# Kernel tuning notes

Measured on AMD Instinct MI355X. Metric: run time of the kernel, lower is better.

Reference implementation:

```python
import jax, jax.numpy as jnp
import numpy as np

EPS = 1e-12


def setup_inputs() -> dict:
    key = jax.random.key(0)
    N, C, H, W = 32, 256, 56, 56
    k1, k2, k3 = jax.random.split(key, 3)
    x = jax.random.normal(k1, (N, C, H, W), dtype=jnp.float32)
    weight = 1.0 + 0.1 * jax.random.normal(k2, (C,), dtype=jnp.float32)
    bias = 0.1 * jax.random.normal(k3, (C,), dtype=jnp.float32)
    # Variable group sizes summing to C=256 (16 groups)
    gs = np.array([8, 24, 8, 16, 32, 16, 8, 8, 16, 24, 8, 16, 16, 8, 32, 16], dtype=np.int64)
    assert gs.sum() == C
    # Per-sample channel permutation expressed as row indices into x.view(N*C, H*W)
    rng = np.random.default_rng(0)
    perms = np.stack([rng.permutation(C) for _ in range(N)])  # [N, C]
    offs = np.arange(N)[:, None] * C
    indexes = (perms + offs).reshape(-1).astype(np.int64)
    inv = np.argsort(perms, axis=1)
    reverse_indexes = (inv + offs).reshape(-1).astype(np.int64)
    return {
        "x": x,
        "weight": weight,
        "bias": bias,
        "group_sizes": jnp.asarray(gs),
        "indexes": jnp.asarray(indexes),
        "reverse_indexes": jnp.asarray(reverse_indexes),
    }


def reference(x, weight, bias, group_sizes, indexes, reverse_indexes):
    N, C, H, W = x.shape
    HW = H * W
    gs = np.asarray(group_sizes)          # static group layout
    G = gs.shape[0]
    seg = jnp.asarray(np.repeat(np.arange(G), gs))  # [C] channel -> group id
    n = jnp.asarray(gs * HW, dtype=x.dtype)         # [G] elements per group

    # gather: per-sample channel permutation
    xg = x.reshape(N * C, HW)[indexes].reshape(N, C, HW)

    # per-group mean via segmented reduction over channels
    s1 = xg.sum(axis=2)                                    # [N, C]
    mu_g = jax.ops.segment_sum(s1.T, seg, num_segments=G).T / n      # [N, G]
    mu_c = mu_g[:, seg]                                    # [N, C]

    diff = xg - mu_c[:, :, None]
    s2 = (diff * diff).sum(axis=2)                         # [N, C]
    # torch.var default is unbiased -> divide by (n - 1)
    var_g = jax.ops.segment_sum(s2.T, seg, num_segments=G).T / (n - 1.0)
    ivar_c = (1.0 / jnp.sqrt(var_g + EPS))[:, seg]         # [N, C]

    out = diff * ivar_c[:, :, None] * weight[None, :, None] + bias[None, :, None]

    # scatter back to original channel order
    out = out.reshape(N * C, HW)[reverse_indexes].reshape(N, C, H, W)
    return out
```

## Files before the change

### kernel.cpp

```cpp
#include <hip/hip_runtime.h>

#define N_ 32
#define C_ 256
#define G_ 16
#define HW_ 3136
#define HW4_ 784
#define EPS_ 1e-12f

typedef float vf4 __attribute__((ext_vector_type(4)));
typedef float vf2 __attribute__((ext_vector_type(2)));

__device__ __forceinline__ int rd_int(const int* __restrict__ p, int i, bool is64) {
    return is64 ? p[2 * i] : p[i];
}

__device__ __forceinline__ void acc4(const vf4 v, float& s, float& s2) {
    s += v.x + v.y + v.z + v.w;
    s2 = fmaf(v.x, v.x, s2);
    s2 = fmaf(v.y, v.y, s2);
    s2 = fmaf(v.z, v.z, s2);
    s2 = fmaf(v.w, v.w, s2);
}

__device__ __forceinline__ vf4 aff(const vf4 v, float sc, float sh) {
    vf4 r;
    r.x = fmaf(v.x, sc, sh);
    r.y = fmaf(v.y, sc, sh);
    r.z = fmaf(v.z, sc, sh);
    r.w = fmaf(v.w, sc, sh);
    return r;
}


__global__ __launch_bounds__(256, 8) void vgn_reduce(
    const float* __restrict__ x,
    const int*   __restrict__ indexes,
    const int*   __restrict__ group_sizes,
    float*       __restrict__ rsums)
{
    const bool is64 = (group_sizes[1] == 0);
    const int t  = threadIdx.x;
    const int r0 = blockIdx.x * 2;

    const int src0 = rd_int(indexes, r0,     is64);
    const int src1 = rd_int(indexes, r0 + 1, is64);
    const vf4* p0 = (const vf4*)x + (size_t)src0 * HW4_;
    const vf4* p1 = (const vf4*)x + (size_t)src1 * HW4_;

    vf4 a0 = p0[t], b0 = p0[t + 256], c0 = p0[t + 512];
    vf4 a1 = p1[t], b1 = p1[t + 256], c1 = p1[t + 512];

    float sA = 0.f, qA = 0.f, sB = 0.f, qB = 0.f;
    if (t < 16) {
        vf4 d0 = p0[768 + t];
        vf4 d1 = p1[768 + t];
        acc4(d0, sA, qA);
        acc4(d1, sB, qB);
    }
    acc4(a0, sA, qA); acc4(b0, sA, qA); acc4(c0, sA, qA);
    acc4(a1, sB, qB); acc4(b1, sB, qB); acc4(c1, sB, qB);

    #pragma unroll
    for (int off = 32; off > 0; off >>= 1) {
        sA += __shfl_down(sA, off);
        qA += __shfl_down(qA, off);
        sB += __shfl_down(sB, off);
        qB += __shfl_down(qB, off);
    }

    __shared__ float red[4][4];
    if ((t & 63) == 0) {
        const int w = t >> 6;
        red[w][0] = sA; red[w][1] = qA; red[w][2] = sB; red[w][3] = qB;
    }
    __syncthreads();
    if (t < 4)
        rsums[r0 * 2 + t] = red[0][t] + red[1][t] + red[2][t] + red[3][t];
}

__global__ __launch_bounds__(256, 8) void vgn_norm(
    const float* __restrict__ x,
    const int*   __restrict__ indexes,
    const int*   __restrict__ group_sizes,
    const float* __restrict__ weight,
    const float* __restrict__ bias,
    const float* __restrict__ rsums,
    float*       __restrict__ out)
{
    const bool is64 = (group_sizes[1] == 0);
    const int t  = threadIdx.x;
    const int r0 = blockIdx.x * 2;
    const int n  = r0 >> 8;

    const int src0 = rd_int(indexes, r0,     is64);
    const int src1 = rd_int(indexes, r0 + 1, is64);
    const vf4* p0 = (const vf4*)x + (size_t)src0 * HW4_;
    const vf4* p1 = (const vf4*)x + (size_t)src1 * HW4_;
    vf4* o0 = (vf4*)out + (size_t)src0 * HW4_;
    vf4* o1 = (vf4*)out + (size_t)src1 * HW4_;

    vf4 a0 = p0[t], b0 = p0[t + 256], c0 = p0[t + 512];
    vf4 a1 = p1[t], b1 = p1[t + 256], c1 = p1[t + 512];
    vf4 d0, d1;
    const bool tail = (t < 16);
    if (tail) { d0 = p0[768 + t]; d1 = p1[768 + t]; }

    __shared__ float sScale[2], sShift[2];
    if (t < 64) {
        const int half = t >> 5;
        const int l    = t & 31;
        const int j    = (r0 + half) & 255;
        int g = 0, P = 0, Pg = 0;
        #pragma unroll
        for (int k = 0; k < G_; k++) {
            P += rd_int(group_sizes, k, is64);
            if (j >= P) { g++; Pg = P; }
        }
        const int gsz = rd_int(group_sizes, g, is64);
        float a = 0.f, b = 0.f;
        if (l < gsz) {
            const vf2 pr = ((const vf2*)rsums)[n * C_ + Pg + l];
            a = pr.x; b = pr.y;
        }
        #pragma unroll
        for (int off = 16; off > 0; off >>= 1) {
            a += __shfl_down(a, off, 32);
            b += __shfl_down(b, off, 32);
        }
        if (l == 0) {
            const float cnt = (float)gsz * (float)HW_;
            const float mu  = a / cnt;
            const float var = (b - mu * a) / (cnt - 1.0f);
            const float ivr = rsqrtf(var + EPS_);
            const float sc  = ivr * weight[j];
            sScale[half] = sc;
            sShift[half] = fmaf(-mu, sc, bias[j]);
        }
    }
    __syncthreads();

    const float sc0 = sScale[0], sh0 = sShift[0];
    const float sc1 = sScale[1], sh1 = sShift[1];

    o0[t]       = aff(a0, sc0, sh0);
    o0[t + 256] = aff(b0, sc0, sh0);
    o0[t + 512] = aff(c0, sc0, sh0);
    o1[t]       = aff(a1, sc1, sh1);
    o1[t + 256] = aff(b1, sc1, sh1);
    o1[t + 512] = aff(c1, sc1, sh1);
    if (tail) {
        o0[768 + t] = aff(d0, sc0, sh0);
        o1[768 + t] = aff(d1, sc1, sh1);
    }
}

extern "C" void kernel_launch(void* const* d_in, const int* in_sizes, int n_in,
                              void* d_out, int out_size, void* d_ws, size_t ws_size,
                              hipStream_t stream) {
    const float* x           = (const float*)d_in[0];
    const float* weight      = (const float*)d_in[1];
    const float* bias        = (const float*)d_in[2];
    const int*   group_sizes = (const int*)  d_in[3];
    const int*   indexes     = (const int*)  d_in[4];

    float* rsums = (float*)d_ws;

    dim3 grid(N_ * C_ / 2), block(256);
    vgn_reduce<<<grid, block, 0, stream>>>(x, indexes, group_sizes, rsums);
    vgn_norm  <<<grid, block, 0, stream>>>(x, indexes, group_sizes,
                                           weight, bias, rsums, (float*)d_out);
}
```

Baseline: 201.9 us.

## Process rows in source order and move group stats into a small kernel

The reduce and normalize kernels now walk x rows contiguously in their original order rather than through the permuted index gather. A new small vgn_stats kernel maps each group's member channels to their source rows via indexes, reduces the per-row sums, and writes per-row scale and shift. The normalize kernel then just loads its two precomputed coefficients. This removes the scattered row access and the per-block group search, at the cost of one more kernel launch.

```diff
diff --git a/kernel.cpp b/kernel.cpp
--- a/kernel.cpp
+++ b/kernel.cpp
@@ -34,18 +34,13 @@
 
 __global__ __launch_bounds__(256, 8) void vgn_reduce(
     const float* __restrict__ x,
-    const int*   __restrict__ indexes,
-    const int*   __restrict__ group_sizes,
     float*       __restrict__ rsums)
 {
-    const bool is64 = (group_sizes[1] == 0);
     const int t  = threadIdx.x;
     const int r0 = blockIdx.x * 2;
 
-    const int src0 = rd_int(indexes, r0,     is64);
-    const int src1 = rd_int(indexes, r0 + 1, is64);
-    const vf4* p0 = (const vf4*)x + (size_t)src0 * HW4_;
-    const vf4* p1 = (const vf4*)x + (size_t)src1 * HW4_;
+    const vf4* p0 = (const vf4*)x + (size_t)r0 * HW4_;
+    const vf4* p1 = p0 + HW4_;
 
     vf4 a0 = p0[t], b0 = p0[t + 256], c0 = p0[t + 512];
     vf4 a1 = p1[t], b1 = p1[t + 256], c1 = p1[t + 512];
@@ -78,26 +73,65 @@
         rsums[r0 * 2 + t] = red[0][t] + red[1][t] + red[2][t] + red[3][t];
 }
 
-__global__ __launch_bounds__(256, 8) void vgn_norm(
-    const float* __restrict__ x,
+__global__ __launch_bounds__(64) void vgn_stats(
     const int*   __restrict__ indexes,
     const int*   __restrict__ group_sizes,
     const float* __restrict__ weight,
     const float* __restrict__ bias,
     const float* __restrict__ rsums,
+    float*       __restrict__ scaleS,
+    float*       __restrict__ shiftS)
+{
+    const bool is64 = (group_sizes[1] == 0);
+    const int n = blockIdx.x >> 4;
+    const int g = blockIdx.x & (G_ - 1);
+    const int l = threadIdx.x;
+
+    int Pg = 0;
+    for (int k = 0; k < g; k++) Pg += rd_int(group_sizes, k, is64);
+    const int gsz = rd_int(group_sizes, g, is64);
+
+    int src = 0;
+    float a = 0.f, b = 0.f;
+    if (l < gsz) {
+        src = rd_int(indexes, n * C_ + Pg + l, is64);
+        const vf2 pr = ((const vf2*)rsums)[src];
+        a = pr.x; b = pr.y;
+    }
+    float A = a, B = b;
+    #pragma unroll
+    for (int off = 32; off > 0; off >>= 1) {
+        A += __shfl_down(A, off);
+        B += __shfl_down(B, off);
+    }
+    A = __shfl(A, 0);
+    B = __shfl(B, 0);
+
+    if (l < gsz) {
+        const float cnt = (float)gsz * (float)HW_;
+        const float mu  = A / cnt;
+        const float var = (B - mu * A) / (cnt - 1.0f);
+        const float ivr = rsqrtf(var + EPS_);
+        const int   c   = Pg + l;
+        const float sc  = ivr * weight[c];
+        scaleS[src] = sc;
+        shiftS[src] = fmaf(-mu, sc, bias[c]);
+    }
+}
+
+__global__ __launch_bounds__(256, 8) void vgn_norm(
+    const float* __restrict__ x,
+    const float* __restrict__ scaleS,
+    const float* __restrict__ shiftS,
     float*       __restrict__ out)
 {
-    const bool is64 = (group_sizes[1] == 0);
     const int t  = threadIdx.x;
     const int r0 = blockIdx.x * 2;
-    const int n  = r0 >> 8;
 
-    const int src0 = rd_int(indexes, r0,     is64);
-    const int src1 = rd_int(indexes, r0 + 1, is64);
-    const vf4* p0 = (const vf4*)x + (size_t)src0 * HW4_;
-    const vf4* p1 = (const vf4*)x + (size_t)src1 * HW4_;
-    vf4* o0 = (vf4*)out + (size_t)src0 * HW4_;
-    vf4* o1 = (vf4*)out + (size_t)src1 * HW4_;
+    const vf4* p0 = (const vf4*)x + (size_t)r0 * HW4_;
+    const vf4* p1 = p0 + HW4_;
+    vf4* o0 = (vf4*)out + (size_t)r0 * HW4_;
+    vf4* o1 = o0 + HW4_;
 
     vf4 a0 = p0[t], b0 = p0[t + 256], c0 = p0[t + 512];
     vf4 a1 = p1[t], b1 = p1[t + 256], c1 = p1[t + 512];
@@ -105,42 +139,8 @@
     const bool tail = (t < 16);
     if (tail) { d0 = p0[768 + t]; d1 = p1[768 + t]; }
 
-    __shared__ float sScale[2], sShift[2];
-    if (t < 64) {
-        const int half = t >> 5;
-        const int l    = t & 31;
-        const int j    = (r0 + half) & 255;
-        int g = 0, P = 0, Pg = 0;
-        #pragma unroll
-        for (int k = 0; k < G_; k++) {
-            P += rd_int(group_sizes, k, is64);
-            if (j >= P) { g++; Pg = P; }
-        }
-        const int gsz = rd_int(group_sizes, g, is64);
-        float a = 0.f, b = 0.f;
-        if (l < gsz) {
-            const vf2 pr = ((const vf2*)rsums)[n * C_ + Pg + l];
-            a = pr.x; b = pr.y;
-        }
-        #pragma unroll
-        for (int off = 16; off > 0; off >>= 1) {
-            a += __shfl_down(a, off, 32);
-            b += __shfl_down(b, off, 32);
-        }
-        if (l == 0) {
-            const float cnt = (float)gsz * (float)HW_;
-            const float mu  = a / cnt;
-            const float var = (b - mu * a) / (cnt - 1.0f);
-            const float ivr = rsqrtf(var + EPS_);
-            const float sc  = ivr * weight[j];
-            sScale[half] = sc;
-            sShift[half] = fmaf(-mu, sc, bias[j]);
-        }
-    }
-    __syncthreads();
-
-    const float sc0 = sScale[0], sh0 = sShift[0];
-    const float sc1 = sScale[1], sh1 = sShift[1];
+    const float sc0 = scaleS[r0],     sh0 = shiftS[r0];
+    const float sc1 = scaleS[r0 + 1], sh1 = shiftS[r0 + 1];
 
     o0[t]       = aff(a0, sc0, sh0);
     o0[t + 256] = aff(b0, sc0, sh0);
@@ -163,10 +163,15 @@
     const int*   group_sizes = (const int*)  d_in[3];
     const int*   indexes     = (const int*)  d_in[4];
 
-    float* rsums = (float*)d_ws;
+    float* rsums  = (float*)d_ws;
+    float* scaleS = (float*)d_ws + 2 * N_ * C_;
+    float* shiftS = scaleS + N_ * C_;
+    float* outp   = (float*)d_out;
 
-    dim3 grid(N_ * C_ / 2), block(256);
-    vgn_reduce<<<grid, block, 0, stream>>>(x, indexes, group_sizes, rsums);
-    vgn_norm  <<<grid, block, 0, stream>>>(x, indexes, group_sizes,
-                                           weight, bias, rsums, (float*)d_out);
+    dim3 blkBulk(256), gridBulk(N_ * C_ / 2);
+    vgn_reduce<<<gridBulk, blkBulk, 0, stream>>>(x, rsums);
+    vgn_stats <<<dim3(N_ * G_), dim3(64), 0, stream>>>(indexes, group_sizes,
+                                                       weight, bias, rsums,
+                                                       scaleS, shiftS);
+    vgn_norm  <<<gridBulk, blkBulk, 0, stream>>>(x, scaleS, shiftS, outp);
 }
```

Measured after the change: 204.6 us. Within noise of the previous version (+1.4%).

## Fuse reduce and normalize into one pass with atomic group barriers

Applied to the files above, without the earlier changes.

Merges the two kernels into one. Each block reduces its two channels, adds the partial sums into per-group atomics, and spins on a flag until the last contributor of the group publishes mean and inverse std. The data stays in registers between reduction and normalization, so x is read once instead of twice. It adds a memset, atomics and spin-waits whose forward progress depends on every block of a group being resident at once.

```diff
diff --git a/kernel.cpp b/kernel.cpp
--- a/kernel.cpp
+++ b/kernel.cpp
@@ -5,10 +5,10 @@
 #define G_ 16
 #define HW_ 3136
 #define HW4_ 784
+#define NG_ (N_ * G_)
 #define EPS_ 1e-12f
 
 typedef float vf4 __attribute__((ext_vector_type(4)));
-typedef float vf2 __attribute__((ext_vector_type(2)));
 
 __device__ __forceinline__ int rd_int(const int* __restrict__ p, int i, bool is64) {
     return is64 ? p[2 * i] : p[i];
@@ -31,29 +31,51 @@
     return r;
 }
 
+__device__ __forceinline__ void vgn_release(
+    float* __restrict__ gS, float* __restrict__ gS2,
+    float* __restrict__ gMu, float* __restrict__ gIv,
+    int* __restrict__ gFlag, int gi, int gsz)
+{
+    const float S = atomicAdd(&gS[gi],  0.0f);
+    const float Q = atomicAdd(&gS2[gi], 0.0f);
+    const float cnt = (float)gsz * (float)HW_;
+    const float mu  = S / cnt;
+    const float var = (Q - mu * S) / (cnt - 1.0f);
+    const float iv  = rsqrtf(var + EPS_);
+    atomicExch(&gMu[gi], mu);
+    atomicExch(&gIv[gi], iv);
+    __threadfence();
+    atomicExch(&gFlag[gi], 1);
+}
 
-__global__ __launch_bounds__(256, 8) void vgn_reduce(
+__global__ __launch_bounds__(256, 8) void vgn_onepass(
     const float* __restrict__ x,
     const int*   __restrict__ indexes,
     const int*   __restrict__ group_sizes,
-    float*       __restrict__ rsums)
+    const float* __restrict__ weight,
+    const float* __restrict__ bias,
+    float* __restrict__ gS,   float* __restrict__ gS2,
+    float* __restrict__ gMu,  float* __restrict__ gIv,
+    int*   __restrict__ gCnt, int*   __restrict__ gFlag,
+    float* __restrict__ out)
 {
     const bool is64 = (group_sizes[1] == 0);
     const int t  = threadIdx.x;
-    const int r0 = blockIdx.x * 2;
+    const int n  = blockIdx.x >> 7;
+    const int p0 = (blockIdx.x & 127) * 2;
 
-    const int src0 = rd_int(indexes, r0,     is64);
-    const int src1 = rd_int(indexes, r0 + 1, is64);
-    const vf4* p0 = (const vf4*)x + (size_t)src0 * HW4_;
-    const vf4* p1 = (const vf4*)x + (size_t)src1 * HW4_;
+    const int src0 = rd_int(indexes, n * C_ + p0,     is64);
+    const int src1 = rd_int(indexes, n * C_ + p0 + 1, is64);
+    const vf4* q0 = (const vf4*)x + (size_t)src0 * HW4_;
+    const vf4* q1 = (const vf4*)x + (size_t)src1 * HW4_;
 
-    vf4 a0 = p0[t], b0 = p0[t + 256], c0 = p0[t + 512];
-    vf4 a1 = p1[t], b1 = p1[t + 256], c1 = p1[t + 512];
+    vf4 a0 = q0[t], b0 = q0[t + 256], c0 = q0[t + 512];
+    vf4 a1 = q1[t], b1 = q1[t + 256], c1 = q1[t + 512];
 
     float sA = 0.f, qA = 0.f, sB = 0.f, qB = 0.f;
     if (t < 16) {
-        vf4 d0 = p0[768 + t];
-        vf4 d1 = p1[768 + t];
+        vf4 d0 = q0[768 + t];
+        vf4 d1 = q1[768 + t];
         acc4(d0, sA, qA);
         acc4(d1, sB, qB);
     }
@@ -69,78 +91,65 @@
     }
 
     __shared__ float red[4][4];
+    __shared__ float sSc[2], sSh[2];
     if ((t & 63) == 0) {
         const int w = t >> 6;
         red[w][0] = sA; red[w][1] = qA; red[w][2] = sB; red[w][3] = qB;
     }
     __syncthreads();
-    if (t < 4)
-        rsums[r0 * 2 + t] = red[0][t] + red[1][t] + red[2][t] + red[3][t];
-}
 
-__global__ __launch_bounds__(256, 8) void vgn_norm(
-    const float* __restrict__ x,
-    const int*   __restrict__ indexes,
-    const int*   __restrict__ group_sizes,
-    const float* __restrict__ weight,
-    const float* __restrict__ bias,
-    const float* __restrict__ rsums,
-    float*       __restrict__ out)
-{
-    const bool is64 = (group_sizes[1] == 0);
-    const int t  = threadIdx.x;
-    const int r0 = blockIdx.x * 2;
-    const int n  = r0 >> 8;
+    if (t == 0) {
+        const float S0 = red[0][0] + red[1][0] + red[2][0] + red[3][0];
+        const float Q0 = red[0][1] + red[1][1] + red[2][1] + red[3][1];
+        const float S1 = red[0][2] + red[1][2] + red[2][2] + red[3][2];
+        const float Q1 = red[0][3] + red[1][3] + red[2][3] + red[3][3];
 
-    const int src0 = rd_int(indexes, r0,     is64);
-    const int src1 = rd_int(indexes, r0 + 1, is64);
-    const vf4* p0 = (const vf4*)x + (size_t)src0 * HW4_;
-    const vf4* p1 = (const vf4*)x + (size_t)src1 * HW4_;
-    vf4* o0 = (vf4*)out + (size_t)src0 * HW4_;
-    vf4* o1 = (vf4*)out + (size_t)src1 * HW4_;
-
-    vf4 a0 = p0[t], b0 = p0[t + 256], c0 = p0[t + 512];
-    vf4 a1 = p1[t], b1 = p1[t + 256], c1 = p1[t + 512];
-    vf4 d0, d1;
-    const bool tail = (t < 16);
-    if (tail) { d0 = p0[768 + t]; d1 = p1[768 + t]; }
-
-    __shared__ float sScale[2], sShift[2];
-    if (t < 64) {
-        const int half = t >> 5;
-        const int l    = t & 31;
-        const int j    = (r0 + half) & 255;
-        int g = 0, P = 0, Pg = 0;
+        int g0 = 0, g1 = 0, P = 0;
         #pragma unroll
         for (int k = 0; k < G_; k++) {
             P += rd_int(group_sizes, k, is64);
-            if (j >= P) { g++; Pg = P; }
+            if (p0     >= P) g0++;
+            if (p0 + 1 >= P) g1++;
         }
-        const int gsz = rd_int(group_sizes, g, is64);
-        float a = 0.f, b = 0.f;
-        if (l < gsz) {
-            const vf2 pr = ((const vf2*)rsums)[n * C_ + Pg + l];
-            a = pr.x; b = pr.y;
+        const int gsz0 = rd_int(group_sizes, g0, is64);
+        const int gsz1 = rd_int(group_sizes, g1, is64);
+        const int gi0 = n * G_ + g0;
+        const int gi1 = n * G_ + g1;
+
+        atomicAdd(&gS[gi0], S0);
+        atomicAdd(&gS2[gi0], Q0);
+        __threadfence();
+        if (atomicAdd(&gCnt[gi0], 1) == gsz0 - 1)
+            vgn_release(gS, gS2, gMu, gIv, gFlag, gi0, gsz0);
+
+        atomicAdd(&gS[gi1], S1);
+        atomicAdd(&gS2[gi1], Q1);
+        __threadfence();
+        if (atomicAdd(&gCnt[gi1], 1) == gsz1 - 1)
+            vgn_release(gS, gS2, gMu, gIv, gFlag, gi1, gsz1);
+
+        while (atomicAdd(&gFlag[gi0], 0) == 0) __builtin_amdgcn_s_sleep(2);
+        const float mu0 = atomicAdd(&gMu[gi0], 0.0f);
+        const float iv0 = atomicAdd(&gIv[gi0], 0.0f);
+        float mu1, iv1;
+        if (gi1 == gi0) { mu1 = mu0; iv1 = iv0; }
+        else {
+            while (atomicAdd(&gFlag[gi1], 0) == 0) __builtin_amdgcn_s_sleep(2);
+            mu1 = atomicAdd(&gMu[gi1], 0.0f);
+            iv1 = atomicAdd(&gIv[gi1], 0.0f);
         }
-        #pragma unroll
-        for (int off = 16; off > 0; off >>= 1) {
-            a += __shfl_down(a, off, 32);
-            b += __shfl_down(b, off, 32);
-        }
-        if (l == 0) {
-            const float cnt = (float)gsz * (float)HW_;
-            const float mu  = a / cnt;
-            const float var = (b - mu * a) / (cnt - 1.0f);
-            const float ivr = rsqrtf(var + EPS_);
-            const float sc  = ivr * weight[j];
-            sScale[half] = sc;
-            sShift[half] = fmaf(-mu, sc, bias[j]);
-        }
+
+        const float sc0 = iv0 * weight[p0];
+        const float sc1 = iv1 * weight[p0 + 1];
+        sSc[0] = sc0; sSh[0] = fmaf(-mu0, sc0, bias[p0]);
+        sSc[1] = sc1; sSh[1] = fmaf(-mu1, sc1, bias[p0 + 1]);
     }
     __syncthreads();
 
-    const float sc0 = sScale[0], sh0 = sShift[0];
-    const float sc1 = sScale[1], sh1 = sShift[1];
+    const float sc0 = sSc[0], sh0 = sSh[0];
+    const float sc1 = sSc[1], sh1 = sSh[1];
+    vf4* o0 = (vf4*)out + (size_t)src0 * HW4_;
+    vf4* o1 = (vf4*)out + (size_t)src1 * HW4_;
 
     o0[t]       = aff(a0, sc0, sh0);
     o0[t + 256] = aff(b0, sc0, sh0);
@@ -148,9 +157,9 @@
     o1[t]       = aff(a1, sc1, sh1);
     o1[t + 256] = aff(b1, sc1, sh1);
     o1[t + 512] = aff(c1, sc1, sh1);
-    if (tail) {
-        o0[768 + t] = aff(d0, sc0, sh0);
-        o1[768 + t] = aff(d1, sc1, sh1);
+    if (t < 16) {
+        o0[768 + t] = aff(q0[768 + t], sc0, sh0);
+        o1[768 + t] = aff(q1[768 + t], sc1, sh1);
     }
 }
 
@@ -163,10 +172,16 @@
     const int*   group_sizes = (const int*)  d_in[3];
     const int*   indexes     = (const int*)  d_in[4];
 
-    float* rsums = (float*)d_ws;
+    float* gS    = (float*)d_ws;
+    float* gS2   = gS  + NG_;
+    float* gMu   = gS2 + NG_;
+    float* gIv   = gMu + NG_;
+    int*   gCnt  = (int*)(gIv + NG_);
+    int*   gFlag = gCnt + NG_;
 
-    dim3 grid(N_ * C_ / 2), block(256);
-    vgn_reduce<<<grid, block, 0, stream>>>(x, indexes, group_sizes, rsums);
-    vgn_norm  <<<grid, block, 0, stream>>>(x, indexes, group_sizes,
-                                           weight, bias, rsums, (float*)d_out);
+    hipMemsetAsync(d_ws, 0, 6 * NG_ * sizeof(float), stream);
+
+    vgn_onepass<<<dim3(N_ * C_ / 2), dim3(256), 0, stream>>>(
+        x, indexes, group_sizes, weight, bias,
+        gS, gS2, gMu, gIv, gCnt, gFlag, (float*)d_out);
 }
```

Result: slower. 528.9 us (+162.0%).
